# Performance work log

Hardware: AMD Instinct MI355X
Metric: run time of the kernel (lower is better)

## Reference

```python
import jax, jax.numpy as jnp
import numpy as np

B, C, H, W = 64, 1, 1024, 1024
G, K, S = 64, 3, 2
HG0, HL = 512, 512
D_IN = K * G * G * C  # 12288


def setup_inputs() -> dict:
    key = jax.random.key(0)
    k1, k2, k3, k4, k5, k6 = jax.random.split(key, 6)
    x = jax.random.normal(k1, (B, C, H, W), dtype=jnp.float32)
    l_t_prev = jax.random.uniform(k2, (B, 2), dtype=jnp.float32, minval=-1.0, maxval=1.0)
    W1 = jax.random.normal(k3, (HG0, D_IN), dtype=jnp.float32) * 0.02
    W2 = jax.random.normal(k4, (HL, 2), dtype=jnp.float32) * 0.02
    W3 = jax.random.normal(k5, (HG0 + HL, HG0), dtype=jnp.float32) * 0.02
    W4 = jax.random.normal(k6, (HG0 + HL, HL), dtype=jnp.float32) * 0.02
    return {"x": x, "l_t_prev": l_t_prev, "W1": W1, "W2": W2, "W3": W3, "W4": W4}


def _extract_patch(x, coords, size):
    """Crop a size x size window per sample, centered at coords, zero-padded OOB,
    then avg-pool by factor size//G down to (B, C, G, G)."""
    r = size // G
    P = size // 2 + 1  # padding used by the torch code; makes every slice in-bounds
    xp = jnp.pad(x, ((0, 0), (0, 0), (P, P), (P, P)))
    sy = coords[:, 1] - size // 2 + P
    sx = coords[:, 0] - size // 2 + P

    def one(im, y0, x0):
        return jax.lax.dynamic_slice(im, (0, y0, x0), (C, size, size))

    p = jax.vmap(one)(xp, sy, sx)  # (B, C, size, size)
    if r > 1:
        p = p.reshape(B, C, G, r, G, r).mean(axis=(3, 5))  # avg_pool2d(kernel=r)
    return p


def _foveate(x, l):
    # denormalize: coords in [0, H], truncated to int
    coords = (0.5 * ((l + 1.0) * H)).astype(jnp.int32)  # (B, 2) as [x, y]
    patches = []
    size = G * S ** (K - 1)
    for _ in range(K):
        patches.append(_extract_patch(x, coords, size))  # (B, 1, G, G)
        size = size // S
    return jnp.concatenate(patches, axis=1)  # (B, K, G, G)


def reference(x, l_t_prev, W1, W2, W3, W4):
    phi = _foveate(x, l_t_prev)                      # (B, K, G, G)
    phi_flat = phi.reshape(phi.shape[0], -1)         # (B, K*G*G)
    h = jax.nn.leaky_relu(phi_flat @ W1.T)           # (B, HG0)
    l_out = jax.nn.leaky_relu(l_t_prev @ W2.T)       # computed but unused (as in source)
    what = h @ W3.T                                  # (B, HG0+HL)
    where = h @ W4.T                                 # fc4 applied to phi features (source quirk)
    g_t = jax.nn.leaky_relu(what + where)
    return g_t
```

## Files before the change

kernel.cpp:

```cpp
#include <hip/hip_runtime.h>
#include <hip/hip_bf16.h>

#define D_IN 12288
#define HG0 512
#define OUT_N 1024

#define KC1 8
#define KSTEPS_BLK 48
#define KSTEPS_WAVE 6

#define NFOV 3072
#define NW34 256

typedef __attribute__((ext_vector_type(8))) short bf16x8;
typedef __attribute__((ext_vector_type(4))) float f32x4;

static __device__ __forceinline__ short f2bf(float f) {
  __hip_bfloat16 h = __float2bfloat16(f);
  return *reinterpret_cast<short*>(&h);
}


__global__ __launch_bounds__(256) void prep_kernel(
    const float* __restrict__ x, const float* __restrict__ l,
    const float* __restrict__ W3, const float* __restrict__ W4,
    short* __restrict__ phis, short* __restrict__ w34s) {
  int bx = blockIdx.x;

  if (bx >= NFOV) {
    int g = (bx - NFOV) * 256 + threadIdx.x;
    float4 a0 = *(const float4*)(W3 + (size_t)g * 8);
    float4 a1 = *(const float4*)(W3 + (size_t)g * 8 + 4);
    float4 b0 = *(const float4*)(W4 + (size_t)g * 8);
    float4 b1 = *(const float4*)(W4 + (size_t)g * 8 + 4);
    int r = g >> 6;
    int c8 = g & 63;
    int ot = r >> 4, lc = r & 15, ks = c8 >> 2, kg = c8 & 3;
    bf16x8 o;
    o[0] = f2bf(a0.x + b0.x); o[1] = f2bf(a0.y + b0.y);
    o[2] = f2bf(a0.z + b0.z); o[3] = f2bf(a0.w + b0.w);
    o[4] = f2bf(a1.x + b1.x); o[5] = f2bf(a1.y + b1.y);
    o[6] = f2bf(a1.z + b1.z); o[7] = f2bf(a1.w + b1.w);
    *(bf16x8*)(w34s + ((((size_t)ot * 16 + ks) * 64) + kg * 16 + lc) * 8) = o;
    return;
  }

  int idx = bx * 256 + threadIdx.x;
  int b = idx / D_IN;
  int d = idx - b * D_IN;
  int k = d >> 12;
  int rem = d & 4095;
  int gy = rem >> 6, gx = rem & 63;

  float lx = l[b * 2 + 0];
  float ly = l[b * 2 + 1];
  int cx = (int)(0.5f * ((lx + 1.0f) * 1024.0f));
  int cy = (int)(0.5f * ((ly + 1.0f) * 1024.0f));

  const float* xb = x + ((size_t)b << 20);
  float v;

  if (k == 0) {
    int y0 = cy - 128 + gy * 4;
    int x0 = cx - 128 + gx * 4;
    float s = 0.0f;
    #pragma unroll
    for (int dy = 0; dy < 4; ++dy) {
      int yy = y0 + dy;
      if ((unsigned)yy < 1024u) {
        const float* row = xb + ((size_t)yy << 10);
        #pragma unroll
        for (int dx = 0; dx < 4; ++dx) {
          int xx = x0 + dx;
          if ((unsigned)xx < 1024u) s += row[xx];
        }
      }
    }
    v = s * 0.0625f;
  } else if (k == 1) {
    int y0 = cy - 64 + gy * 2;
    int x0 = cx - 64 + gx * 2;
    float s = 0.0f;
    #pragma unroll
    for (int dy = 0; dy < 2; ++dy) {
      int yy = y0 + dy;
      if ((unsigned)yy < 1024u) {
        const float* row = xb + ((size_t)yy << 10);
        #pragma unroll
        for (int dx = 0; dx < 2; ++dx) {
          int xx = x0 + dx;
          if ((unsigned)xx < 1024u) s += row[xx];
        }
      }
    }
    v = s * 0.25f;
  } else {
    int yy = cy - 32 + gy;
    int xx = cx - 32 + gx;
    v = 0.0f;
    if ((unsigned)yy < 1024u && (unsigned)xx < 1024u) v = xb[((size_t)yy << 10) + xx];
  }

  int ks = d >> 5, kg = (d >> 3) & 3, e = d & 7, t = b >> 4, lcb = b & 15;
  phis[(((size_t)ks * 4 + t) * 64 + kg * 16 + lcb) * 8 + e] = f2bf(v);
}

__global__ __launch_bounds__(512) void gemm1_kernel(
    const short* __restrict__ phis, const float* __restrict__ W1,
    float* __restrict__ partial1) {
  __shared__ __align__(16) char smem[KSTEPS_BLK * 64 * 8 * 2];
  float* lds_o = (float*)smem;

  int tid = threadIdx.x;
  int wave = tid >> 6;
  int lane = tid & 63;
  int lc = lane & 15, kg = lane >> 4;
  int jt = blockIdx.x;
  int kc = blockIdx.y;
  int j0 = jt * 16;

  {
    int r = tid >> 5;
    int c32 = tid & 31;
    const float* row = W1 + (size_t)(j0 + r) * D_IN + (size_t)kc * (KSTEPS_BLK * 32);
    int kgc = (c32 >> 1) & 3;
    int e0 = (c32 & 1) * 4;
    #pragma unroll
    for (int q = 0; q < 12; ++q) {
      int c = (c32 + q * 32) * 4;
      int ks = (c32 >> 3) + 4 * q;
      float4 v = *(const float4*)(row + c);
      short4 s4;
      s4.x = f2bf(v.x); s4.y = f2bf(v.y); s4.z = f2bf(v.z); s4.w = f2bf(v.w);
      int byte = ((ks * 64 + kgc * 16 + r) * 16 + e0 * 2) ^ ((ks & 7) << 4);
      *(short4*)(smem + byte) = s4;
    }
  }
  __syncthreads();

  f32x4 acc[4] = {{0,0,0,0},{0,0,0,0},{0,0,0,0},{0,0,0,0}};
  int ksw = wave * KSTEPS_WAVE;
  const short* pbase = phis + (((size_t)kc * KSTEPS_BLK + ksw) * 4 * 64 + lane) * 8;

  #pragma unroll
  for (int s = 0; s < KSTEPS_WAVE; ++s) {
    int ks = ksw + s;
    int abyte = ((ks * 64 + lane) * 16) ^ ((ks & 7) << 4);
    bf16x8 af = *(const bf16x8*)(smem + abyte);
    #pragma unroll
    for (int t = 0; t < 4; ++t) {
      bf16x8 bf = *(const bf16x8*)(pbase + ((size_t)s * 4 + t) * 512);
      acc[t] = __builtin_amdgcn_mfma_f32_16x16x32_bf16(af, bf, acc[t], 0, 0, 0);
    }
  }
  __syncthreads();

  #pragma unroll
  for (int t = 0; t < 4; ++t)
    #pragma unroll
    for (int r = 0; r < 4; ++r)
      lds_o[wave * 1024 + (kg * 4 + r) * 64 + t * 16 + lc] = acc[t][r];
  __syncthreads();

  float* pp = partial1 + (size_t)kc * (HG0 * 64) + (size_t)jt * 1024;
  #pragma unroll
  for (int i = 0; i < 2; ++i) {
    int e = tid + 512 * i;
    float s = 0.0f;
    #pragma unroll
    for (int w = 0; w < 8; ++w) s += lds_o[w * 1024 + e];
    pp[e] = s;
  }
}

__global__ __launch_bounds__(256) void reduce1_kernel(
    const float* __restrict__ partial1, short* __restrict__ hs) {
  int idx = blockIdx.x * 256 + threadIdx.x;
  float s = 0.0f;
  #pragma unroll
  for (int kc = 0; kc < KC1; ++kc) s += partial1[(size_t)kc * (HG0 * 64) + idx];
  float v = (s >= 0.0f) ? s : 0.01f * s;
  int j = idx >> 6, b = idx & 63;
  int ks = j >> 5, kg = (j >> 3) & 3, e = j & 7, t = b >> 4, lc = b & 15;
  hs[(((size_t)ks * 4 + t) * 64 + kg * 16 + lc) * 8 + e] = f2bf(v);
}

__global__ __launch_bounds__(256) void gemm2_kernel(
    const short* __restrict__ hs, const short* __restrict__ w34s,
    float* __restrict__ out) {
  __shared__ float lds[4 * 1024];
  int wave = threadIdx.x >> 6;
  int lane = threadIdx.x & 63;
  int lc = lane & 15, kg = lane >> 4;
  int ot = blockIdx.x;
  int o0 = ot * 16;

  f32x4 acc[4] = {{0,0,0,0},{0,0,0,0},{0,0,0,0},{0,0,0,0}};

  #pragma unroll
  for (int ksl = 0; ksl < 4; ++ksl) {
    int kstep = wave * 4 + ksl;
    bf16x8 bfr = *(const bf16x8*)(w34s + (((size_t)ot * 16 + kstep) * 64 + lane) * 8);
    #pragma unroll
    for (int t = 0; t < 4; ++t) {
      bf16x8 af = *(const bf16x8*)(hs + (((size_t)kstep * 4 + t) * 64 + lane) * 8);
      acc[t] = __builtin_amdgcn_mfma_f32_16x16x32_bf16(af, bfr, acc[t], 0, 0, 0);
    }
  }

  #pragma unroll
  for (int t = 0; t < 4; ++t)
    #pragma unroll
    for (int r = 0; r < 4; ++r)
      lds[wave * 1024 + t * 256 + kg * 64 + r * 16 + lc] = acc[t][r];
  __syncthreads();

  #pragma unroll
  for (int i = 0; i < 4; ++i) {
    int e = threadIdx.x + 256 * i;
    float s = lds[e] + lds[1024 + e] + lds[2048 + e] + lds[3072 + e];
    float v = (s >= 0.0f) ? s : 0.01f * s;
    int b = ((e >> 8) << 4) + (((e >> 6) & 3) << 2) + ((e >> 4) & 3);
    out[(size_t)b * OUT_N + o0 + (e & 15)] = v;
  }
}

extern "C" void kernel_launch(void* const* d_in, const int* in_sizes, int n_in,
                              void* d_out, int out_size, void* d_ws, size_t ws_size,
                              hipStream_t stream) {
  const float* x  = (const float*)d_in[0];
  const float* l  = (const float*)d_in[1];
  const float* W1 = (const float*)d_in[2];
  const float* W3 = (const float*)d_in[4];
  const float* W4 = (const float*)d_in[5];
  float* out = (float*)d_out;

  char* ws = (char*)d_ws;
  short* phis     = (short*)(ws);
  float* partial1 = (float*)(ws + (2u << 20));
  short* hs       = (short*)(ws + (5u << 20));
  short* w34s     = (short*)(ws + (6u << 20));

  prep_kernel<<<dim3(NFOV + NW34), dim3(256), 0, stream>>>(x, l, W3, W4, phis, w34s);
  gemm1_kernel<<<dim3(32, KC1), dim3(512), 0, stream>>>(phis, W1, partial1);
  reduce1_kernel<<<dim3((HG0 * 64) / 256), dim3(256), 0, stream>>>(partial1, hs);
  gemm2_kernel<<<dim3(OUT_N / 16), dim3(256), 0, stream>>>(hs, w34s, out);
}
```

Baseline: 27.72 us.

## Fuse split-K reduction into second GEMM kernel, recomputing h per block

Removes the separate reduce1 kernel. Each of the 64 gemm2 blocks now re-reads all eight split-K partial sums of h, applies leaky ReLU, and writes h as bf16 into LDS before running the MFMA GEMM with 8 waves. This saves one kernel launch and the hs global round trip. In exchange, every block redundantly reads the full 1 MB partial buffer, so L2 traffic grows, and the block now uses 64 KB of LDS.

```diff
diff --git a/kernel.cpp b/kernel.cpp
--- a/kernel.cpp
+++ b/kernel.cpp
@@ -173,52 +173,68 @@
   }
 }
 
-__global__ __launch_bounds__(256) void reduce1_kernel(
-    const float* __restrict__ partial1, short* __restrict__ hs) {
-  int idx = blockIdx.x * 256 + threadIdx.x;
-  float s = 0.0f;
-  #pragma unroll
-  for (int kc = 0; kc < KC1; ++kc) s += partial1[(size_t)kc * (HG0 * 64) + idx];
-  float v = (s >= 0.0f) ? s : 0.01f * s;
-  int j = idx >> 6, b = idx & 63;
-  int ks = j >> 5, kg = (j >> 3) & 3, e = j & 7, t = b >> 4, lc = b & 15;
-  hs[(((size_t)ks * 4 + t) * 64 + kg * 16 + lc) * 8 + e] = f2bf(v);
-}
-
-__global__ __launch_bounds__(256) void gemm2_kernel(
-    const short* __restrict__ hs, const short* __restrict__ w34s,
+__global__ __launch_bounds__(512) void gemm2r_kernel(
+    const float* __restrict__ partial1, const short* __restrict__ w34s,
     float* __restrict__ out) {
-  __shared__ float lds[4 * 1024];
-  int wave = threadIdx.x >> 6;
-  int lane = threadIdx.x & 63;
+  __shared__ __align__(16) char smem[65536];
+  short* hs = (short*)smem;
+  float* lds_o = (float*)smem;
+
+  int tid = threadIdx.x;
+  int wave = tid >> 6;
+  int lane = tid & 63;
   int lc = lane & 15, kg = lane >> 4;
   int ot = blockIdx.x;
   int o0 = ot * 16;
 
+  #pragma unroll
+  for (int q = 0; q < 16; ++q) {
+    int i4 = q * 512 + tid;
+    f32x4 s = {0, 0, 0, 0};
+    #pragma unroll
+    for (int kc = 0; kc < KC1; ++kc) {
+      float4 v = *(const float4*)(partial1 + (size_t)kc * (HG0 * 64) + (size_t)i4 * 4);
+      s[0] += v.x; s[1] += v.y; s[2] += v.z; s[3] += v.w;
+    }
+    int idx0 = i4 * 4;
+    #pragma unroll
+    for (int u = 0; u < 4; ++u) {
+      int idx = idx0 + u;
+      float vv = s[u];
+      vv = (vv >= 0.0f) ? vv : 0.01f * vv;
+      int j = idx >> 6, b = idx & 63;
+      int ks = j >> 5, kgg = (j >> 3) & 3, e = j & 7, t = b >> 4, lcc = b & 15;
+      hs[((ks * 4 + t) * 64 + kgg * 16 + lcc) * 8 + e] = f2bf(vv);
+    }
+  }
+  __syncthreads();
+
   f32x4 acc[4] = {{0,0,0,0},{0,0,0,0},{0,0,0,0},{0,0,0,0}};
-
-  #pragma unroll
-  for (int ksl = 0; ksl < 4; ++ksl) {
-    int kstep = wave * 4 + ksl;
+  #pragma unroll
+  for (int ksl = 0; ksl < 2; ++ksl) {
+    int kstep = wave * 2 + ksl;
     bf16x8 bfr = *(const bf16x8*)(w34s + (((size_t)ot * 16 + kstep) * 64 + lane) * 8);
     #pragma unroll
     for (int t = 0; t < 4; ++t) {
-      bf16x8 af = *(const bf16x8*)(hs + (((size_t)kstep * 4 + t) * 64 + lane) * 8);
+      bf16x8 af = *(const bf16x8*)(hs + ((size_t)(kstep * 4 + t) * 64 + lane) * 8);
       acc[t] = __builtin_amdgcn_mfma_f32_16x16x32_bf16(af, bfr, acc[t], 0, 0, 0);
     }
   }
+  __syncthreads();
 
   #pragma unroll
   for (int t = 0; t < 4; ++t)
     #pragma unroll
     for (int r = 0; r < 4; ++r)
-      lds[wave * 1024 + t * 256 + kg * 64 + r * 16 + lc] = acc[t][r];
-  __syncthreads();
-
-  #pragma unroll
-  for (int i = 0; i < 4; ++i) {
-    int e = threadIdx.x + 256 * i;
-    float s = lds[e] + lds[1024 + e] + lds[2048 + e] + lds[3072 + e];
+      lds_o[wave * 1024 + t * 256 + kg * 64 + r * 16 + lc] = acc[t][r];
+  __syncthreads();
+
+  #pragma unroll
+  for (int i = 0; i < 2; ++i) {
+    int e = tid + 512 * i;
+    float s = 0.0f;
+    #pragma unroll
+    for (int w = 0; w < 8; ++w) s += lds_o[w * 1024 + e];
     float v = (s >= 0.0f) ? s : 0.01f * s;
     int b = ((e >> 8) << 4) + (((e >> 6) & 3) << 2) + ((e >> 4) & 3);
     out[(size_t)b * OUT_N + o0 + (e & 15)] = v;
@@ -238,11 +254,9 @@
   char* ws = (char*)d_ws;
   short* phis     = (short*)(ws);
   float* partial1 = (float*)(ws + (2u << 20));
-  short* hs       = (short*)(ws + (5u << 20));
   short* w34s     = (short*)(ws + (6u << 20));
 
   prep_kernel<<<dim3(NFOV + NW34), dim3(256), 0, stream>>>(x, l, W3, W4, phis, w34s);
   gemm1_kernel<<<dim3(32, KC1), dim3(512), 0, stream>>>(phis, W1, partial1);
-  reduce1_kernel<<<dim3((HG0 * 64) / 256), dim3(256), 0, stream>>>(partial1, hs);
-  gemm2_kernel<<<dim3(OUT_N / 16), dim3(256), 0, stream>>>(hs, w34s, out);
-}
+  gemm2r_kernel<<<dim3(OUT_N / 16), dim3(512), 0, stream>>>(partial1, w34s, out);
+}
```

Measured after the change: 34.33 us. 1.24x slower.
